# Optimization experiments

Measured on AMD Instinct MI355X. Metric: run time of the kernel, lower is better.

## Reference

```python
import jax, jax.numpy as jnp
import numpy as np

NUM_TRACKS = [5313, 1643, 128, 0]
MAX_TRACKS = max(NUM_TRACKS)
EMBED_DIM = 1536
LN_EPS = 1e-5


def setup_inputs() -> dict:
    key = jax.random.key(0)
    ks = jax.random.split(key, 8)
    B, S, D = 4, 896, EMBED_DIM
    inp = {
        "x": jax.random.normal(ks[0], (B, S, D), dtype=jnp.float32),
        "head_idx": jax.random.randint(ks[1], (B,), 0, 4, dtype=jnp.int64) if jax.config.jax_enable_x64 else jax.random.randint(ks[1], (B,), 0, 4).astype(jnp.int32),
    }
    for i, n in enumerate([5313, 1643, 128]):
        inp[f"gamma{i}"] = jnp.ones((D,), jnp.float32)
        inp[f"beta{i}"] = jnp.zeros((D,), jnp.float32)
        inp[f"W{i}"] = jax.random.normal(ks[2 + i], (n, D), dtype=jnp.float32) * 0.02
        inp[f"b{i}"] = jnp.zeros((n,), jnp.float32)
    return inp


def _linear_head(x, gamma, beta, W, b):
    # LayerNormFP32 -> Linear -> softplus, cast back to orig dtype
    orig_dtype = x.dtype
    xf = x.astype(jnp.float32)
    mu = jnp.mean(xf, axis=-1, keepdims=True)
    var = jnp.var(xf, axis=-1, keepdims=True)  # biased, as torch LayerNorm
    xn = (xf - mu) * jax.lax.rsqrt(var + LN_EPS) * gamma + beta
    h = jax.nn.softplus(jnp.einsum("bsd,td->bst", xn, W) + b)
    return h.astype(orig_dtype)


def reference(x, head_idx, gamma0, beta0, W0, b0,
              gamma1, beta1, W1, b1, gamma2, beta2, W2, b2):
    params = [(gamma0, beta0, W0, b0),
              (gamma1, beta1, W1, b1),
              (gamma2, beta2, W2, b2),
              None]  # ZeroHead
    B, S, _ = x.shape
    logits = jnp.zeros((B, S, MAX_TRACKS), dtype=x.dtype)
    for i, p in enumerate(params):
        if p is None:
            padded = jnp.zeros((B, S, MAX_TRACKS), dtype=x.dtype)
        else:
            h = _linear_head(x, *p)  # [B, S, n_i]
            pad = MAX_TRACKS - h.shape[-1]
            padded = jnp.pad(h, ((0, 0), (0, 0), (0, pad))) if pad > 0 else h
        mask = (head_idx == i)[:, None, None]
        logits = jnp.where(mask, padded, logits)
    return logits
```

## Files before the change

### kernel.cpp

```cpp
#include <hip/hip_runtime.h>
#include <hip/hip_bf16.h>

#define EMBED 1536
#define SEQ   896
#define NOUT  5313

#define N0 5313
#define N1 1643
#define N2 128
#define W0OFF 0
#define W1OFF 5376
#define W2OFF 7040
#define PTOT  7168

#define LN_BLOCKS 1792
#define WC_BLOCKS 5376
#define MT64 14
#define GEMM_GRID 2352

typedef __attribute__((ext_vector_type(8))) short bf16x8;
typedef __attribute__((ext_vector_type(4))) float f32x4;

__device__ __forceinline__ void gload_lds16(const void* g, void* l) {
    __builtin_amdgcn_global_load_lds(
        (const __attribute__((address_space(1))) void*)g,
        (__attribute__((address_space(3))) void*)l, 16, 0, 0);
}

__device__ __forceinline__ int tiles_of(int h) {
    return (h == 0) ? 42 : (h == 1) ? 13 : (h == 2) ? 1 : 0;
}
__device__ __forceinline__ int nrows_of(int h) {
    return (h == 0) ? N0 : (h == 1) ? N1 : (h == 2) ? N2 : 0;
}

__global__ __launch_bounds__(256) void prep_kernel(
    const float* __restrict__ x, const int* __restrict__ head_idx,
    const float* __restrict__ g0, const float* __restrict__ be0,
    const float* __restrict__ g1, const float* __restrict__ be1,
    const float* __restrict__ g2, const float* __restrict__ be2,
    const float* __restrict__ W0, const float* __restrict__ W1,
    const float* __restrict__ W2,
    __hip_bfloat16* __restrict__ xn, __hip_bfloat16* __restrict__ wpad)
{
    const int tid = threadIdx.x;

    if (blockIdx.x < LN_BLOCKS) {
        const int half = tid >> 7;
        const int lt   = tid & 127;
        const int row  = blockIdx.x * 2 + half;
        const int b    = row / SEQ;
        const int h    = head_idx[b];
        if (h == 3) return;

        const float* gamma = (h == 1) ? g1 : (h == 2) ? g2 : g0;
        const float* beta  = (h == 1) ? be1 : (h == 2) ? be2 : be0;
        const float* xr = x + (size_t)row * EMBED;

        float4 v[3];
        float sum = 0.f, sq = 0.f;
#pragma unroll
        for (int i = 0; i < 3; ++i) {
            v[i] = ((const float4*)xr)[lt + i * 128];
            sum += v[i].x + v[i].y + v[i].z + v[i].w;
            sq  += v[i].x * v[i].x + v[i].y * v[i].y + v[i].z * v[i].z + v[i].w * v[i].w;
        }
#pragma unroll
        for (int off = 32; off > 0; off >>= 1) {
            sum += __shfl_down(sum, off);
            sq  += __shfl_down(sq, off);
        }
        __shared__ float s_sum[4], s_sq[4];
        const int wave = tid >> 6, lane = tid & 63;
        if (lane == 0) { s_sum[wave] = sum; s_sq[wave] = sq; }
        __syncthreads();
        const int wb = half << 1;
        const float mu  = (s_sum[wb] + s_sum[wb + 1]) * (1.f / EMBED);
        const float var = (s_sq[wb] + s_sq[wb + 1]) * (1.f / EMBED) - mu * mu;
        const float rs  = rsqrtf(var + 1e-5f);

        __hip_bfloat16* xo = xn + (size_t)row * EMBED;
#pragma unroll
        for (int i = 0; i < 3; ++i) {
            const int idx = lt + i * 128;
            float4 gv = ((const float4*)gamma)[idx];
            float4 bv = ((const float4*)beta)[idx];
            union { __hip_bfloat16 h4[4]; short4 s4; } u;
            u.h4[0] = __float2bfloat16((v[i].x - mu) * rs * gv.x + bv.x);
            u.h4[1] = __float2bfloat16((v[i].y - mu) * rs * gv.y + bv.y);
            u.h4[2] = __float2bfloat16((v[i].z - mu) * rs * gv.z + bv.z);
            u.h4[3] = __float2bfloat16((v[i].w - mu) * rs * gv.w + bv.w);
            ((short4*)xo)[idx] = u.s4;
        }
    } else {
        const int gid = (blockIdx.x - LN_BLOCKS) * 256 + tid;
        const int r = gid / 192;
        const int c = (gid - r * 192) * 8;
        const int region = (r < W1OFF) ? 0 : (r < W2OFF) ? 1 : 2;
        const int h0 = head_idx[0], h1 = head_idx[1];
        const int h2 = head_idx[2], h3 = head_idx[3];
        if (region != h0 && region != h1 && region != h2 && region != h3)
            return;
        const float* src = nullptr;
        if (region == 0)      { if (r < N0) src = W0 + (size_t)r * EMBED; }
        else if (region == 1) { int rr = r - W1OFF; if (rr < N1) src = W1 + (size_t)rr * EMBED; }
        else                  { int rr = r - W2OFF; if (rr < N2) src = W2 + (size_t)rr * EMBED; }
        union { __hip_bfloat16 h8[8]; int4 v4; } u;
        if (src) {
            float4 a = ((const float4*)(src + c))[0];
            float4 b = ((const float4*)(src + c))[1];
            u.h8[0] = __float2bfloat16(a.x); u.h8[1] = __float2bfloat16(a.y);
            u.h8[2] = __float2bfloat16(a.z); u.h8[3] = __float2bfloat16(a.w);
            u.h8[4] = __float2bfloat16(b.x); u.h8[5] = __float2bfloat16(b.y);
            u.h8[6] = __float2bfloat16(b.z); u.h8[7] = __float2bfloat16(b.w);
        } else {
            u.v4 = make_int4(0, 0, 0, 0);
        }
        *(int4*)(wpad + (size_t)r * EMBED + c) = u.v4;
    }
}

__global__ __launch_bounds__(256, 2) void head_gemm(
    const __hip_bfloat16* __restrict__ xn,
    const __hip_bfloat16* __restrict__ wpad,
    const float* __restrict__ b0, const float* __restrict__ b1,
    const float* __restrict__ b2,
    const int* __restrict__ head_idx,
    float* __restrict__ out)
{
    const int h0 = head_idx[0], h1 = head_idx[1];
    const int h2 = head_idx[2], h3 = head_idx[3];
    const int t0 = tiles_of(h0) * MT64, t1 = tiles_of(h1) * MT64;
    const int t2 = tiles_of(h2) * MT64, t3 = tiles_of(h3) * MT64;
    const int R = t0 + t1 + t2 + t3;
    const int tid = threadIdx.x;

    if ((int)blockIdx.x >= R) {
        const int j = blockIdx.x - R;
        const int ZB = GEMM_GRID - R;
        for (int row = j; row < 4 * SEQ; row += ZB) {
            const int b = row / SEQ;
            const int h = (b == 0) ? h0 : (b == 1) ? h1 : (b == 2) ? h2 : h3;
            const int n = nrows_of(h);
            if (n >= NOUT) continue;
            float* o = out + (size_t)row * NOUT;
            const int pre0 = (4 - (int)(((size_t)row * NOUT + n) & 3)) & 3;
            const int pre_end = min(n + pre0, NOUT);
            for (int c = n + tid; c < pre_end; c += 256) o[c] = 0.f;
            const int nvec = (NOUT - pre_end) >> 2;
            const float4 z = make_float4(0.f, 0.f, 0.f, 0.f);
            float4* ov = (float4*)(o + pre_end);
            for (int i = tid; i < nvec; i += 256) ov[i] = z;
            for (int c = pre_end + (nvec << 2) + tid; c < NOUT; c += 256) o[c] = 0.f;
        }
        return;
    }

    int rem = blockIdx.x, b;
    if (rem < t0)           { b = 0; }
    else if (rem < t0 + t1) { b = 1; rem -= t0; }
    else if (rem < t0 + t1 + t2) { b = 2; rem -= t0 + t1; }
    else                    { b = 3; rem -= t0 + t1 + t2; }

    const int h = (b == 0) ? h0 : (b == 1) ? h1 : (b == 2) ? h2 : h3;
    const int ntc = tiles_of(h);
    const int mt = rem / ntc;
    const int nt = rem - mt * ntc;
    const int nrows = nrows_of(h);
    const int wbase = (h == 0) ? W0OFF : (h == 1) ? W1OFF : W2OFF;

    const int col0 = nt * 128;
    float* outb = out + ((size_t)b * SEQ + (size_t)mt * 64) * NOUT;

    __shared__ __hip_bfloat16 As[64 * 64];
    __shared__ __hip_bfloat16 Bs[128 * 64];
    const __hip_bfloat16* Ab = xn + ((size_t)b * SEQ + (size_t)mt * 64) * EMBED;
    const __hip_bfloat16* Bb = wpad + (size_t)(wbase + col0) * EMBED;

    const int wave = tid >> 6, lane = tid & 63;
    const int wm = wave >> 1, wn = wave & 1;
    const int fm = lane & 15, quad = lane >> 4;
    const int fsw = fm & 7;

    f32x4 acc[2][4] = {};

    for (int kt = 0; kt < EMBED / 64; ++kt) {
        const int k0 = kt * 64;
        __syncthreads();
#pragma unroll
        for (int i = 0; i < 2; ++i) {
            const int c = tid + i * 256;
            const int arow = c >> 3;
            const int kc = (c & 7) ^ (arow & 7);
            gload_lds16(Ab + (size_t)arow * EMBED + k0 + kc * 8, As + c * 8);
        }
#pragma unroll
        for (int i = 0; i < 4; ++i) {
            const int c = tid + i * 256;
            const int brow = c >> 3;
            const int kc = (c & 7) ^ (brow & 7);
            gload_lds16(Bb + (size_t)brow * EMBED + k0 + kc * 8, Bs + c * 8);
        }
        __syncthreads();
#pragma unroll
        for (int ks = 0; ks < 2; ++ks) {
            bf16x8 af[2], bfr[4];
#pragma unroll
            for (int i = 0; i < 2; ++i)
                af[i] = *(const bf16x8*)&As[(wm * 32 + i * 16 + fm) * 64 +
                                            (((ks << 2) + quad) ^ fsw) * 8];
#pragma unroll
            for (int j = 0; j < 4; ++j)
                bfr[j] = *(const bf16x8*)&Bs[(wn * 64 + j * 16 + fm) * 64 +
                                             (((ks << 2) + quad) ^ fsw) * 8];
#pragma unroll
            for (int i = 0; i < 2; ++i)
#pragma unroll
                for (int j = 0; j < 4; ++j)
                    acc[i][j] = __builtin_amdgcn_mfma_f32_16x16x32_bf16(
                        af[i], bfr[j], acc[i][j], 0, 0, 0);
        }
    }

    const float* bias = (h == 1) ? b1 : (h == 2) ? b2 : b0;
#pragma unroll
    for (int j = 0; j < 4; ++j) {
        const int lcol = col0 + wn * 64 + j * 16 + fm;
        const bool valid = lcol < nrows;
        const float bv = valid ? bias[lcol] : 0.f;
#pragma unroll
        for (int i = 0; i < 2; ++i) {
            const int rbase = wm * 32 + i * 16 + quad * 4;
#pragma unroll
            for (int r = 0; r < 4; ++r) {
                const float v = acc[i][j][r] + bv;
                const float sp = fmaxf(v, 0.f) + __logf(1.f + __expf(-fabsf(v)));
                if (valid) outb[(size_t)(rbase + r) * NOUT + lcol] = sp;
            }
        }
    }
}

extern "C" void kernel_launch(void* const* d_in, const int* in_sizes, int n_in,
                              void* d_out, int out_size, void* d_ws, size_t ws_size,
                              hipStream_t stream) {
    const float* x   = (const float*)d_in[0];
    const int* hidx  = (const int*)d_in[1];
    const float* g0  = (const float*)d_in[2];
    const float* be0 = (const float*)d_in[3];
    const float* W0  = (const float*)d_in[4];
    const float* b0  = (const float*)d_in[5];
    const float* g1  = (const float*)d_in[6];
    const float* be1 = (const float*)d_in[7];
    const float* W1  = (const float*)d_in[8];
    const float* b1  = (const float*)d_in[9];
    const float* g2  = (const float*)d_in[10];
    const float* be2 = (const float*)d_in[11];
    const float* W2  = (const float*)d_in[12];
    const float* b2  = (const float*)d_in[13];
    float* out = (float*)d_out;

    const size_t XN_BYTES = (size_t)4 * SEQ * EMBED * 2;
    __hip_bfloat16* xn   = (__hip_bfloat16*)d_ws;
    __hip_bfloat16* wpad = (__hip_bfloat16*)((char*)d_ws + XN_BYTES);

    prep_kernel<<<LN_BLOCKS + WC_BLOCKS, 256, 0, stream>>>(
        x, hidx, g0, be0, g1, be1, g2, be2, W0, W1, W2, xn, wpad);
    head_gemm<<<GEMM_GRID, 256, 0, stream>>>(xn, wpad, b0, b1, b2, hidx, out);
}
```

Baseline: 175.5 us.

## Fuse prep and GEMM into one persistent cooperative kernel with grid sync

```diff
diff --git a/kernel.cpp b/kernel.cpp
--- a/kernel.cpp
+++ b/kernel.cpp
@@ -1,5 +1,8 @@
 #include <hip/hip_runtime.h>
 #include <hip/hip_bf16.h>
+#include <hip/hip_cooperative_groups.h>
+
+namespace cg = cooperative_groups;
 
 #define EMBED 1536
 #define SEQ   896
@@ -13,10 +16,10 @@
 #define W2OFF 7040
 #define PTOT  7168
 
-#define LN_BLOCKS 1792
-#define WC_BLOCKS 5376
+#define GRID 512
+#define LN_PAIRS 1792
+#define WC_ITERS 5376
 #define MT64 14
-#define GEMM_GRID 2352
 
 typedef __attribute__((ext_vector_type(8))) short bf16x8;
 typedef __attribute__((ext_vector_type(4))) float f32x4;
@@ -34,24 +37,31 @@
     return (h == 0) ? N0 : (h == 1) ? N1 : (h == 2) ? N2 : 0;
 }
 
-__global__ __launch_bounds__(256) void prep_kernel(
+__global__ __launch_bounds__(256, 2) void fused_kernel(
     const float* __restrict__ x, const int* __restrict__ head_idx,
     const float* __restrict__ g0, const float* __restrict__ be0,
     const float* __restrict__ g1, const float* __restrict__ be1,
     const float* __restrict__ g2, const float* __restrict__ be2,
     const float* __restrict__ W0, const float* __restrict__ W1,
     const float* __restrict__ W2,
-    __hip_bfloat16* __restrict__ xn, __hip_bfloat16* __restrict__ wpad)
+    const float* __restrict__ b0, const float* __restrict__ b1,
+    const float* __restrict__ b2,
+    __hip_bfloat16* __restrict__ xn, __hip_bfloat16* __restrict__ wpad,
+    float* __restrict__ out)
 {
     const int tid = threadIdx.x;
-
-    if (blockIdx.x < LN_BLOCKS) {
+    const int h0 = head_idx[0], h1 = head_idx[1];
+    const int h2 = head_idx[2], h3 = head_idx[3];
+
+    __shared__ float s_sum[4], s_sq[4];
+
+    for (int pr = blockIdx.x; pr < LN_PAIRS; pr += GRID) {
         const int half = tid >> 7;
         const int lt   = tid & 127;
-        const int row  = blockIdx.x * 2 + half;
+        const int row  = pr * 2 + half;
         const int b    = row / SEQ;
-        const int h    = head_idx[b];
-        if (h == 3) return;
+        const int h    = (b == 0) ? h0 : (b == 1) ? h1 : (b == 2) ? h2 : h3;
+        if (h == 3) continue;
 
         const float* gamma = (h == 1) ? g1 : (h == 2) ? g2 : g0;
         const float* beta  = (h == 1) ? be1 : (h == 2) ? be2 : be0;
@@ -70,7 +80,6 @@
             sum += __shfl_down(sum, off);
             sq  += __shfl_down(sq, off);
         }
-        __shared__ float s_sum[4], s_sq[4];
         const int wave = tid >> 6, lane = tid & 63;
         if (lane == 0) { s_sum[wave] = sum; s_sq[wave] = sq; }
         __syncthreads();
@@ -92,15 +101,16 @@
             u.h4[3] = __float2bfloat16((v[i].w - mu) * rs * gv.w + bv.w);
             ((short4*)xo)[idx] = u.s4;
         }
-    } else {
-        const int gid = (blockIdx.x - LN_BLOCKS) * 256 + tid;
+        __syncthreads();
+    }
+
+    for (int cb = blockIdx.x; cb < WC_ITERS; cb += GRID) {
+        const int gid = cb * 256 + tid;
         const int r = gid / 192;
         const int c = (gid - r * 192) * 8;
         const int region = (r < W1OFF) ? 0 : (r < W2OFF) ? 1 : 2;
-        const int h0 = head_idx[0], h1 = head_idx[1];
-        const int h2 = head_idx[2], h3 = head_idx[3];
         if (region != h0 && region != h1 && region != h2 && region != h3)
-            return;
+            continue;
         const float* src = nullptr;
         if (region == 0)      { if (r < N0) src = W0 + (size_t)r * EMBED; }
         else if (region == 1) { int rr = r - W1OFF; if (rr < N1) src = W1 + (size_t)rr * EMBED; }
@@ -118,126 +128,115 @@
         }
         *(int4*)(wpad + (size_t)r * EMBED + c) = u.v4;
     }
-}
-
-__global__ __launch_bounds__(256, 2) void head_gemm(
-    const __hip_bfloat16* __restrict__ xn,
-    const __hip_bfloat16* __restrict__ wpad,
-    const float* __restrict__ b0, const float* __restrict__ b1,
-    const float* __restrict__ b2,
-    const int* __restrict__ head_idx,
-    float* __restrict__ out)
-{
-    const int h0 = head_idx[0], h1 = head_idx[1];
-    const int h2 = head_idx[2], h3 = head_idx[3];
+
+    for (int row = blockIdx.x; row < 4 * SEQ; row += GRID) {
+        const int b = row / SEQ;
+        const int h = (b == 0) ? h0 : (b == 1) ? h1 : (b == 2) ? h2 : h3;
+        const int n = nrows_of(h);
+        if (n >= NOUT) continue;
+        float* o = out + (size_t)row * NOUT;
+        const int pre0 = (4 - (int)(((size_t)row * NOUT + n) & 3)) & 3;
+        const int pre_end = min(n + pre0, NOUT);
+        for (int c = n + tid; c < pre_end; c += 256) o[c] = 0.f;
+        const int nvec = (NOUT - pre_end) >> 2;
+        const float4 z = make_float4(0.f, 0.f, 0.f, 0.f);
+        float4* ov = (float4*)(o + pre_end);
+        for (int i = tid; i < nvec; i += 256) ov[i] = z;
+        for (int c = pre_end + (nvec << 2) + tid; c < NOUT; c += 256) o[c] = 0.f;
+    }
+
+    __threadfence();
+    cg::this_grid().sync();
+
     const int t0 = tiles_of(h0) * MT64, t1 = tiles_of(h1) * MT64;
     const int t2 = tiles_of(h2) * MT64, t3 = tiles_of(h3) * MT64;
     const int R = t0 + t1 + t2 + t3;
-    const int tid = threadIdx.x;
-
-    if ((int)blockIdx.x >= R) {
-        const int j = blockIdx.x - R;
-        const int ZB = GEMM_GRID - R;
-        for (int row = j; row < 4 * SEQ; row += ZB) {
-            const int b = row / SEQ;
-            const int h = (b == 0) ? h0 : (b == 1) ? h1 : (b == 2) ? h2 : h3;
-            const int n = nrows_of(h);
-            if (n >= NOUT) continue;
-            float* o = out + (size_t)row * NOUT;
-            const int pre0 = (4 - (int)(((size_t)row * NOUT + n) & 3)) & 3;
-            const int pre_end = min(n + pre0, NOUT);
-            for (int c = n + tid; c < pre_end; c += 256) o[c] = 0.f;
-            const int nvec = (NOUT - pre_end) >> 2;
-            const float4 z = make_float4(0.f, 0.f, 0.f, 0.f);
-            float4* ov = (float4*)(o + pre_end);
-            for (int i = tid; i < nvec; i += 256) ov[i] = z;
-            for (int c = pre_end + (nvec << 2) + tid; c < NOUT; c += 256) o[c] = 0.f;
-        }
-        return;
-    }
-
-    int rem = blockIdx.x, b;
-    if (rem < t0)           { b = 0; }
-    else if (rem < t0 + t1) { b = 1; rem -= t0; }
-    else if (rem < t0 + t1 + t2) { b = 2; rem -= t0 + t1; }
-    else                    { b = 3; rem -= t0 + t1 + t2; }
-
-    const int h = (b == 0) ? h0 : (b == 1) ? h1 : (b == 2) ? h2 : h3;
-    const int ntc = tiles_of(h);
-    const int mt = rem / ntc;
-    const int nt = rem - mt * ntc;
-    const int nrows = nrows_of(h);
-    const int wbase = (h == 0) ? W0OFF : (h == 1) ? W1OFF : W2OFF;
-
-    const int col0 = nt * 128;
-    float* outb = out + ((size_t)b * SEQ + (size_t)mt * 64) * NOUT;
 
     __shared__ __hip_bfloat16 As[64 * 64];
     __shared__ __hip_bfloat16 Bs[128 * 64];
-    const __hip_bfloat16* Ab = xn + ((size_t)b * SEQ + (size_t)mt * 64) * EMBED;
-    const __hip_bfloat16* Bb = wpad + (size_t)(wbase + col0) * EMBED;
 
     const int wave = tid >> 6, lane = tid & 63;
     const int wm = wave >> 1, wn = wave & 1;
     const int fm = lane & 15, quad = lane >> 4;
     const int fsw = fm & 7;
 
-    f32x4 acc[2][4] = {};
-
-    for (int kt = 0; kt < EMBED / 64; ++kt) {
-        const int k0 = kt * 64;
+    for (int id = blockIdx.x; id < R; id += GRID) {
+        int rem = id, b;
+        if (rem < t0)                { b = 0; }
+        else if (rem < t0 + t1)      { b = 1; rem -= t0; }
+        else if (rem < t0 + t1 + t2) { b = 2; rem -= t0 + t1; }
+        else                         { b = 3; rem -= t0 + t1 + t2; }
+
+        const int h = (b == 0) ? h0 : (b == 1) ? h1 : (b == 2) ? h2 : h3;
+        const int ntc = tiles_of(h);
+        const int mt = rem / ntc;
+        const int nt = rem - mt * ntc;
+        const int nrows = nrows_of(h);
+        const int wbase = (h == 0) ? W0OFF : (h == 1) ? W1OFF : W2OFF;
+
+        const int col0 = nt * 128;
+        float* outb = out + ((size_t)b * SEQ + (size_t)mt * 64) * NOUT;
+        const __hip_bfloat16* Ab = xn + ((size_t)b * SEQ + (size_t)mt * 64) * EMBED;
+        const __hip_bfloat16* Bb = wpad + (size_t)(wbase + col0) * EMBED;
+
+        f32x4 acc[2][4] = {};
+
+        for (int kt = 0; kt < EMBED / 64; ++kt) {
+            const int k0 = kt * 64;
+            __syncthreads();
+#pragma unroll
+            for (int i = 0; i < 2; ++i) {
+                const int c = tid + i * 256;
+                const int arow = c >> 3;
+                const int kc = (c & 7) ^ (arow & 7);
+                gload_lds16(Ab + (size_t)arow * EMBED + k0 + kc * 8, As + c * 8);
+            }
+#pragma unroll
+            for (int i = 0; i < 4; ++i) {
+                const int c = tid + i * 256;
+                const int brow = c >> 3;
+                const int kc = (c & 7) ^ (brow & 7);
+                gload_lds16(Bb + (size_t)brow * EMBED + k0 + kc * 8, Bs + c * 8);
+            }
+            __syncthreads();
+#pragma unroll
+            for (int ks = 0; ks < 2; ++ks) {
+                bf16x8 af[2], bfr[4];
+#pragma unroll
+                for (int i = 0; i < 2; ++i)
+                    af[i] = *(const bf16x8*)&As[(wm * 32 + i * 16 + fm) * 64 +
+                                                (((ks << 2) + quad) ^ fsw) * 8];
+#pragma unroll
+                for (int j = 0; j < 4; ++j)
+                    bfr[j] = *(const bf16x8*)&Bs[(wn * 64 + j * 16 + fm) * 64 +
+                                                 (((ks << 2) + quad) ^ fsw) * 8];
+#pragma unroll
+                for (int i = 0; i < 2; ++i)
+#pragma unroll
+                    for (int j = 0; j < 4; ++j)
+                        acc[i][j] = __builtin_amdgcn_mfma_f32_16x16x32_bf16(
+                            af[i], bfr[j], acc[i][j], 0, 0, 0);
+            }
+        }
+
+        const float* bias = (h == 1) ? b1 : (h == 2) ? b2 : b0;
+#pragma unroll
+        for (int j = 0; j < 4; ++j) {
+            const int lcol = col0 + wn * 64 + j * 16 + fm;
+            const bool valid = lcol < nrows;
+            const float bv = valid ? bias[lcol] : 0.f;
+#pragma unroll
+            for (int i = 0; i < 2; ++i) {
+                const int rbase = wm * 32 + i * 16 + quad * 4;
+#pragma unroll
+                for (int r = 0; r < 4; ++r) {
+                    const float v = acc[i][j][r] + bv;
+                    const float sp = fmaxf(v, 0.f) + __logf(1.f + __expf(-fabsf(v)));
+                    if (valid) outb[(size_t)(rbase + r) * NOUT + lcol] = sp;
+                }
+            }
+        }
         __syncthreads();
-#pragma unroll
-        for (int i = 0; i < 2; ++i) {
-            const int c = tid + i * 256;
-            const int arow = c >> 3;
-            const int kc = (c & 7) ^ (arow & 7);
-            gload_lds16(Ab + (size_t)arow * EMBED + k0 + kc * 8, As + c * 8);
-        }
-#pragma unroll
-        for (int i = 0; i < 4; ++i) {
-            const int c = tid + i * 256;
-            const int brow = c >> 3;
-            const int kc = (c & 7) ^ (brow & 7);
-            gload_lds16(Bb + (size_t)brow * EMBED + k0 + kc * 8, Bs + c * 8);
-        }
-        __syncthreads();
-#pragma unroll
-        for (int ks = 0; ks < 2; ++ks) {
-            bf16x8 af[2], bfr[4];
-#pragma unroll
-            for (int i = 0; i < 2; ++i)
-                af[i] = *(const bf16x8*)&As[(wm * 32 + i * 16 + fm) * 64 +
-                                            (((ks << 2) + quad) ^ fsw) * 8];
-#pragma unroll
-            for (int j = 0; j < 4; ++j)
-                bfr[j] = *(const bf16x8*)&Bs[(wn * 64 + j * 16 + fm) * 64 +
-                                             (((ks << 2) + quad) ^ fsw) * 8];
-#pragma unroll
-            for (int i = 0; i < 2; ++i)
-#pragma unroll
-                for (int j = 0; j < 4; ++j)
-                    acc[i][j] = __builtin_amdgcn_mfma_f32_16x16x32_bf16(
-                        af[i], bfr[j], acc[i][j], 0, 0, 0);
-        }
-    }
-
-    const float* bias = (h == 1) ? b1 : (h == 2) ? b2 : b0;
-#pragma unroll
-    for (int j = 0; j < 4; ++j) {
-        const int lcol = col0 + wn * 64 + j * 16 + fm;
-        const bool valid = lcol < nrows;
-        const float bv = valid ? bias[lcol] : 0.f;
-#pragma unroll
-        for (int i = 0; i < 2; ++i) {
-            const int rbase = wm * 32 + i * 16 + quad * 4;
-#pragma unroll
-            for (int r = 0; r < 4; ++r) {
-                const float v = acc[i][j][r] + bv;
-                const float sp = fmaxf(v, 0.f) + __logf(1.f + __expf(-fabsf(v)));
-                if (valid) outb[(size_t)(rbase + r) * NOUT + lcol] = sp;
-            }
-        }
     }
 }
 
@@ -264,7 +263,13 @@
     __hip_bfloat16* xn   = (__hip_bfloat16*)d_ws;
     __hip_bfloat16* wpad = (__hip_bfloat16*)((char*)d_ws + XN_BYTES);
 
-    prep_kernel<<<LN_BLOCKS + WC_BLOCKS, 256, 0, stream>>>(
-        x, hidx, g0, be0, g1, be1, g2, be2, W0, W1, W2, xn, wpad);
-    head_gemm<<<GEMM_GRID, 256, 0, stream>>>(xn, wpad, b0, b1, b2, hidx, out);
-}
+    void* args[] = {
+        (void*)&x, (void*)&hidx,
+        (void*)&g0, (void*)&be0, (void*)&g1, (void*)&be1, (void*)&g2, (void*)&be2,
+        (void*)&W0, (void*)&W1, (void*)&W2,
+        (void*)&b0, (void*)&b1, (void*)&b2,
+        (void*)&xn, (void*)&wpad, (void*)&out
+    };
+    hipLaunchCooperativeKernel((const void*)fused_kernel,
+                               dim3(GRID), dim3(256), args, 0, stream);
+}
```

Measured after the change: 341.4 us. 94.5% more time.
